# Performance work log

Measured on AMD Instinct MI355X. Metric: run time of the kernel, lower is better.

The kernel has to match this reference:

```python
import jax, jax.numpy as jnp
import numpy as np

BATCH, SEQ, DIM, HEADS, DSTATE, BLOCK = 2, 4096, 1024, 16, 64, 64
LN_EPS = 1e-6

def segsum(x):
    # x: (..., T) -> (..., T, T); segsum[i, j] = sum_{j < k <= i} x[k]; -inf above diagonal
    T = x.shape[-1]
    cs = jnp.cumsum(x, axis=-1)
    seg = cs[..., :, None] - cs[..., None, :]
    mask = jnp.tril(jnp.ones((T, T), dtype=bool))
    return jnp.where(mask, seg, -jnp.inf)

def ssd_minimal_discrete(X, A, C, B, block_len):
    # X: (b,s,h,p) already multiplied by dt; A: (b,s,h) = A*dt; C readout, B input: (b,s,h,n)
    b, s, h, p = X.shape
    n = B.shape[-1]
    c = s // block_len
    l = block_len
    Xc = X.reshape(b, c, l, h, p)
    Bc = B.reshape(b, c, l, h, n)
    Cc = C.reshape(b, c, l, h, n)
    Ac = A.reshape(b, c, l, h).transpose(0, 3, 1, 2)  # (b,h,c,l)
    A_cumsum = jnp.cumsum(Ac, axis=-1)
    # 1. intra-chunk (diagonal block) outputs
    L = jnp.exp(segsum(Ac))  # (b,h,c,l,l)
    Y_diag = jnp.einsum('bclhn,bcshn,bhcls,bcshp->bclhp', Cc, Bc, L, Xc)
    # 2. states at end of each chunk
    decay_states = jnp.exp(A_cumsum[..., -1:] - A_cumsum)
    states = jnp.einsum('bclhn,bhcl,bclhp->bchpn', Bc, decay_states, Xc)
    # 3. inter-chunk recurrence on chunk states
    init = jnp.zeros_like(states[:, :1])
    states = jnp.concatenate([init, states], axis=1)  # (b,c+1,h,p,n)
    decay_chunk = jnp.exp(segsum(jnp.pad(A_cumsum[..., -1], ((0, 0), (0, 0), (1, 0)))))
    new_states = jnp.einsum('bhzc,bchpn->bzhpn', decay_chunk, states)
    states, final_state = new_states[:, :-1], new_states[:, -1]
    # 4. state -> output contribution (off-diagonal blocks)
    state_decay_out = jnp.exp(A_cumsum)
    Y_off = jnp.einsum('bclhn,bchpn,bhcl->bclhp', Cc, states, state_decay_out)
    return (Y_diag + Y_off).reshape(b, s, h, p), final_state

def setup_inputs():
    key = jax.random.key(0)
    ks = jax.random.split(key, 8)
    X = jax.random.normal(ks[0], (BATCH, SEQ, DIM), jnp.float32)
    B = jax.random.normal(ks[1], (BATCH, SEQ, HEADS * DSTATE), jnp.float32)
    C = jax.random.normal(ks[2], (BATCH, SEQ, HEADS * DSTATE), jnp.float32)
    W_dt = jax.random.normal(ks[3], (DIM, HEADS), jnp.float32) * 0.02
    # dt_bias initializer: inverse-softplus of dt ~ LogUniform(1e-3, 1e-1)
    dt = jnp.exp(jax.random.uniform(ks[4], (1, SEQ, HEADS)) * (jnp.log(0.1) - jnp.log(0.001)) + jnp.log(0.001))
    dt = jnp.clip(dt, 1e-4)
    dt_bias = dt + jnp.log(-jnp.expm1(-dt))
    # a_log initializer: log of Uniform(1, 16)
    a_log = jnp.log(jax.random.uniform(ks[5], (HEADS,), minval=1.0, maxval=16.0))
    W_out = jax.random.normal(ks[6], (DIM, DIM), jnp.float32) * 0.02
    ln_scale = jnp.ones((DIM,), jnp.float32)
    ln_bias = jnp.zeros((DIM,), jnp.float32)
    return {"X": X, "B": B, "C": C, "W_dt": W_dt, "dt_bias": dt_bias, "a_log": a_log,
            "W_out": W_out, "ln_scale": ln_scale, "ln_bias": ln_bias, "block_len": BLOCK}

def reference(X, B, C, W_dt, dt_bias, a_log, W_out, ln_scale, ln_bias, block_len):
    b, s, dim = X.shape
    h = a_log.shape[0]
    Xh = X.reshape(b, s, h, -1)
    Bh = B.reshape(b, s, h, -1)
    Ch = C.reshape(b, s, h, -1)
    dt = jax.nn.softplus(jnp.einsum('bsd,dh->bsh', X, W_dt) + dt_bias)  # (b,s,h)
    A = -jnp.exp(a_log)  # (h,)
    y, final_state = ssd_minimal_discrete(Xh * dt[..., None], A * dt, Ch, Bh, block_len)
    y = y.reshape(b, s, dim)
    mu = jnp.mean(y, axis=-1, keepdims=True)
    var = jnp.mean(jnp.square(y - mu), axis=-1, keepdims=True)
    yn = (y - mu) / jnp.sqrt(var + LN_EPS) * ln_scale + ln_bias
    out = jnp.einsum('bsd,de->bse', yn, W_out)
    return out, final_state
```

## Files before the change

kernel.cpp:

```cpp
#include <hip/hip_runtime.h>
#include <hip/hip_bf16.h>
#include <hip/hip_fp16.h>
#include <math.h>

#define BATCH   2
#define SEQ     4096
#define DIM     1024
#define HEADS   16
#define DSTATE  64
#define HEADDIM 64
#define BLOCKL  64
#define NCHUNK  64
#define ROWS    (BATCH*SEQ)

typedef __attribute__((ext_vector_type(4))) float f32x4;
typedef __attribute__((ext_vector_type(8))) short bf16x8;
typedef __attribute__((ext_vector_type(8))) _Float16 f16x8;

static __device__ __forceinline__ float softplus_f(float x){
    return (x > 20.f) ? x : log1pf(__expf(x));
}
static __device__ __forceinline__ ushort f2b(float f){
    __hip_bfloat16 h = __float2bfloat16(f);
    return *reinterpret_cast<ushort*>(&h);
}
static __device__ __forceinline__ float b2f(ushort u){
    uint x = ((uint)u) << 16;
    return *reinterpret_cast<float*>(&x);
}
static __device__ __forceinline__ void gload16(const void* g, void* l){
    __builtin_amdgcn_global_load_lds((const __attribute__((address_space(1))) unsigned int*)g,
                                     (__attribute__((address_space(3))) unsigned int*)l, 16, 0, 0);
}

__global__ __launch_bounds__(256) void k_dtwt(const float* __restrict__ X,
        const float* __restrict__ Wdt, const float* __restrict__ dtb,
        const float* __restrict__ alog, const float* __restrict__ W,
        float* __restrict__ dt_g, float* __restrict__ dtA_g,
        ushort* __restrict__ Wt){
    __shared__ float xrow[DIM];
    __shared__ float red[16][17];
    __shared__ float t[64][65];
    int bidx = blockIdx.x;
    int tid = threadIdx.x;
    if (bidx < ROWS){
        int r = bidx;
        int s = r & (SEQ-1);
        *(f32x4*)(xrow + tid*4) = *(const f32x4*)(X + (size_t)r*DIM + tid*4);
        __syncthreads();
        int part = tid >> 4, h = tid & 15;
        int d0 = part * 64;
        float acc = 0.f;
        #pragma unroll 8
        for (int i = 0; i < 64; ++i)
            acc += xrow[d0 + i] * Wdt[(size_t)(d0 + i)*HEADS + h];
        red[part][h] = acc;
        __syncthreads();
        if (tid < 16){
            float sum = 0.f;
            #pragma unroll
            for (int p = 0; p < 16; ++p) sum += red[p][tid];
            sum += dtb[(size_t)s*HEADS + tid];
            float dtv = softplus_f(sum);
            dt_g[(size_t)r*HEADS + tid]  = dtv;
            dtA_g[(size_t)r*HEADS + tid] = -__expf(alog[tid]) * dtv;
        }
    } else {
        int bid = bidx - ROWS;
        int kt = bid >> 4, nt = bid & 15;
        int lr = tid >> 4, lc4 = (tid & 15) * 4;
        #pragma unroll
        for (int q = 0; q < 4; ++q){
            int k = lr + q*16;
            *(f32x4*)&t[k][lc4] = *(const f32x4*)(W + (size_t)(kt*64 + k)*DIM + nt*64 + lc4);
        }
        __syncthreads();
        #pragma unroll
        for (int q = 0; q < 4; ++q){
            int n = lr + q*16;
            ushort o[4];
            #pragma unroll
            for (int j = 0; j < 4; ++j) o[j] = f2b(t[lc4+j][n]);
            *(short4*)(Wt + (size_t)(nt*64 + n)*DIM + kt*64 + lc4) = *(short4*)&o[0];
        }
    }
}

__global__ __launch_bounds__(256) void k_chunk(const float* __restrict__ X,
        const float* __restrict__ Bin, const float* __restrict__ Cin,
        const float* __restrict__ dt_g, const float* __restrict__ dtA_g,
        ushort* __restrict__ ybf, ushort* __restrict__ cstate, float* __restrict__ css_g){
    int bid = blockIdx.x;
    int h = bid & 15, c = (bid >> 4) & 63, b = bid >> 10;
    int tid = threadIdx.x;
    int lane = tid & 63, wave = tid >> 6;
    int r0 = b*SEQ + c*BLOCKL;

    __shared__ __align__(16) char region0[18432];
    __shared__ __align__(16) ushort WBT[64*72];
    __shared__ float csh[64], dtsh[64], wsh[64];
    ushort* Cs  = (ushort*)region0;
    ushort* Bs  = (ushort*)(region0 + 9216);
    ushort* Mb  = (ushort*)region0;
    ushort* XdT = (ushort*)(region0 + 9216);

    int l  = tid >> 2;
    int c0 = (tid & 3) * 16;

    f32x4 xr[4], br[4], cr[4];
    {
        const float* xp = X   + (size_t)(r0 + l)*DIM + h*HEADDIM + c0;
        const float* bp = Bin + (size_t)(r0 + l)*DIM + h*DSTATE  + c0;
        const float* cp = Cin + (size_t)(r0 + l)*DIM + h*DSTATE  + c0;
        #pragma unroll
        for (int q = 0; q < 4; ++q){
            xr[q] = *(const f32x4*)(xp + q*4);
            br[q] = *(const f32x4*)(bp + q*4);
            cr[q] = *(const f32x4*)(cp + q*4);
        }
    }
    if (tid < 64){
        dtsh[tid] = dt_g[(size_t)(r0 + tid)*HEADS + h];
        float a = dtA_g[(size_t)(r0 + tid)*HEADS + h];
        #pragma unroll
        for (int off = 1; off < 64; off <<= 1){
            float v = __shfl_up(a, off, 64);
            if (tid >= off) a += v;
        }
        csh[tid] = a;
        css_g[(size_t)bid*64 + tid] = a;
        float cs63 = __shfl(a, 63, 64);
        wsh[tid] = __expf(cs63 - a);
    }
    {
        ushort tc[16], tb[16];
        #pragma unroll
        for (int q = 0; q < 4; ++q)
            #pragma unroll
            for (int j = 0; j < 4; ++j){
                tc[q*4+j] = f2b(cr[q][j]);
                tb[q*4+j] = f2b(br[q][j]);
            }
        *(uint4*)&Cs[l*72 + c0]     = *(uint4*)&tc[0];
        *(uint4*)&Cs[l*72 + c0 + 8] = *(uint4*)&tc[8];
        *(uint4*)&Bs[l*72 + c0]     = *(uint4*)&tb[0];
        *(uint4*)&Bs[l*72 + c0 + 8] = *(uint4*)&tb[8];
    }
    __syncthreads();

    int cl15  = lane & 15;
    int g     = lane >> 4;
    int arow  = wave*16 + cl15;
    int kof   = g * 8;
    int rbase = wave*16 + g*4;

    {
        float wl = wsh[l];
        #pragma unroll
        for (int q = 0; q < 4; ++q)
            #pragma unroll
            for (int j = 0; j < 4; ++j)
                WBT[(c0 + q*4 + j)*72 + l] = f2b(br[q][j] * wl);
    }
    f32x4 gacc[4];
    #pragma unroll
    for (int j = 0; j < 4; ++j) gacc[j] = (f32x4){0.f,0.f,0.f,0.f};
    #pragma unroll
    for (int k = 0; k < 2; ++k){
        bf16x8 a = *(const bf16x8*)&Cs[arow*72 + k*32 + kof];
        #pragma unroll
        for (int j = 0; j < 4; ++j){
            bf16x8 bb = *(const bf16x8*)&Bs[(16*j + cl15)*72 + k*32 + kof];
            gacc[j] = __builtin_amdgcn_mfma_f32_16x16x32_bf16(a, bb, gacc[j], 0, 0, 0);
        }
    }
    __syncthreads();

    #pragma unroll
    for (int j = 0; j < 4; ++j){
        #pragma unroll
        for (int r = 0; r < 4; ++r){
            int row = rbase + r, col = 16*j + cl15;
            float m = 0.f;
            if (col <= row) m = gacc[j][r] * __expf(csh[row] - csh[col]);
            Mb[row*72 + col] = f2b(m);
        }
    }
    {
        float dl = dtsh[l];
        #pragma unroll
        for (int q = 0; q < 4; ++q)
            #pragma unroll
            for (int j = 0; j < 4; ++j)
                XdT[(c0 + q*4 + j)*72 + l] = f2b(xr[q][j] * dl);
    }
    __syncthreads();

    f32x4 y[4];
    #pragma unroll
    for (int j = 0; j < 4; ++j) y[j] = (f32x4){0.f,0.f,0.f,0.f};
    #pragma unroll
    for (int k = 0; k < 2; ++k){
        bf16x8 am = *(const bf16x8*)&Mb[arow*72 + k*32 + kof];
        #pragma unroll
        for (int j = 0; j < 4; ++j){
            bf16x8 bx = *(const bf16x8*)&XdT[(16*j + cl15)*72 + k*32 + kof];
            y[j] = __builtin_amdgcn_mfma_f32_16x16x32_bf16(am, bx, y[j], 0, 0, 0);
        }
    }
    #pragma unroll
    for (int j = 0; j < 4; ++j)
        #pragma unroll
        for (int r = 0; r < 4; ++r)
            ybf[(size_t)(r0 + rbase + r)*DIM + h*HEADDIM + 16*j + cl15] = f2b(y[j][r]);

    f32x4 st[4];
    #pragma unroll
    for (int j = 0; j < 4; ++j) st[j] = (f32x4){0.f,0.f,0.f,0.f};
    #pragma unroll
    for (int k = 0; k < 2; ++k){
        bf16x8 aw = *(const bf16x8*)&XdT[arow*72 + k*32 + kof];
        #pragma unroll
        for (int j = 0; j < 4; ++j){
            bf16x8 bb = *(const bf16x8*)&WBT[(16*j + cl15)*72 + k*32 + kof];
            st[j] = __builtin_amdgcn_mfma_f32_16x16x32_bf16(aw, bb, st[j], 0, 0, 0);
        }
    }
    #pragma unroll
    for (int j = 0; j < 4; ++j)
        #pragma unroll
        for (int r = 0; r < 4; ++r){
            __half hv = __float2half(st[j][r]);
            cstate[(size_t)bid*4096 + (size_t)(rbase + r)*64 + 16*j + cl15] = *(ushort*)&hv;
        }
}

__global__ __launch_bounds__(256) void k_scan(ushort* __restrict__ cstate,
        const float* __restrict__ css_g, float* __restrict__ fs_out){
    int bid = blockIdx.x;
    int tile = bid & 7, hh = (bid >> 3) & 15, b = bid >> 7;
    int pn = tile*512 + threadIdx.x*2;
    size_t base0 = (size_t)(b*NCHUNK)*HEADS + hh;
    float P0 = 0.f, P1 = 0.f;
    __half2 cur = *(const __half2*)&cstate[base0*4096 + pn];
    for (int c = 0; c < NCHUNK; ++c){
        size_t base = base0 + (size_t)c*HEADS;
        __half2 nxt = cur;
        if (c < NCHUNK-1) nxt = *(const __half2*)&cstate[(base + HEADS)*4096 + pn];
        float e = __expf(css_g[base*64 + 63]);
        *( __half2*)&cstate[base*4096 + pn] = __floats2half2_rn(P0, P1);
        float2 cf = __half22float2(cur);
        P0 = e*P0 + cf.x;
        P1 = e*P1 + cf.y;
        cur = nxt;
    }
    *(float2*)&fs_out[(size_t)(b*HEADS + hh)*4096 + pn] = make_float2(P0, P1);
}

__global__ __launch_bounds__(256) void k_yoff(const float* __restrict__ Cin,
        const ushort* __restrict__ cstate, const float* __restrict__ css_g,
        ushort* __restrict__ ybf){
    int bid = blockIdx.x;
    int h = bid & 15, c = (bid >> 4) & 63, b = bid >> 10;
    int tid = threadIdx.x;
    int lane = tid & 63, wave = tid >> 6;
    int r0 = b*SEQ + c*BLOCKL;
    __shared__ __align__(16) ushort Cs[64*72];
    __shared__ __align__(16) ushort Ss[64*72];
    __shared__ float cse[64];
    {
        int l  = tid >> 2;
        int c0 = (tid & 3) * 16;
        const float* cp = Cin + (size_t)(r0 + l)*DIM + h*DSTATE + c0;
        ushort tc[16];
        #pragma unroll
        for (int q = 0; q < 4; ++q){
            f32x4 vc = *(const f32x4*)(cp + q*4);
            #pragma unroll
            for (int j = 0; j < 4; ++j){
                __half hv = __float2half(vc[j]);
                tc[q*4+j] = *(ushort*)&hv;
            }
        }
        *(uint4*)&Cs[l*72 + c0]     = *(uint4*)&tc[0];
        *(uint4*)&Cs[l*72 + c0 + 8] = *(uint4*)&tc[8];
        const ushort* sp = cstate + (size_t)bid*4096 + (size_t)l*64 + c0;
        *(uint4*)&Ss[l*72 + c0]     = *(const uint4*)sp;
        *(uint4*)&Ss[l*72 + c0 + 8] = *(const uint4*)(sp + 8);
    }
    if (tid < 64) cse[tid] = __expf(css_g[(size_t)bid*64 + tid]);
    __syncthreads();

    int cl15 = lane & 15;
    int g    = lane >> 4;
    int arow = wave*16 + cl15;
    int kof  = g * 8;
    f32x4 acc[4];
    #pragma unroll
    for (int j = 0; j < 4; ++j) acc[j] = (f32x4){0.f,0.f,0.f,0.f};
    #pragma unroll
    for (int k = 0; k < 2; ++k){
        f16x8 a = *(const f16x8*)&Cs[arow*72 + k*32 + kof];
        #pragma unroll
        for (int j = 0; j < 4; ++j){
            f16x8 bb = *(const f16x8*)&Ss[(16*j + cl15)*72 + k*32 + kof];
            acc[j] = __builtin_amdgcn_mfma_f32_16x16x32_f16(a, bb, acc[j], 0, 0, 0);
        }
    }
    int rbase = wave*16 + g*4;
    #pragma unroll
    for (int j = 0; j < 4; ++j)
        #pragma unroll
        for (int r = 0; r < 4; ++r){
            float e = cse[rbase + r];
            size_t idx = (size_t)(r0 + rbase + r)*DIM + h*HEADDIM + 16*j + cl15;
            ybf[idx] = f2b(b2f(ybf[idx]) + e * acc[j][r]);
        }
}

__global__ __launch_bounds__(256) void k_ln(ushort* __restrict__ ybf,
        const float* __restrict__ scale, const float* __restrict__ bias){
    int r = blockIdx.x, tid = threadIdx.x;
    ushort* yp = ybf + (size_t)r*DIM + tid*4;
    short4 raw = *(const short4*)yp;
    float v[4];
    v[0] = b2f((ushort)raw.x); v[1] = b2f((ushort)raw.y);
    v[2] = b2f((ushort)raw.z); v[3] = b2f((ushort)raw.w);
    float s1 = v[0]+v[1]+v[2]+v[3];
    float s2 = v[0]*v[0]+v[1]*v[1]+v[2]*v[2]+v[3]*v[3];
    #pragma unroll
    for (int m = 32; m > 0; m >>= 1){
        s1 += __shfl_xor(s1, m, 64);
        s2 += __shfl_xor(s2, m, 64);
    }
    __shared__ float w1[4], w2[4];
    int wv = tid >> 6;
    if ((tid & 63) == 0){ w1[wv] = s1; w2[wv] = s2; }
    __syncthreads();
    float S1 = w1[0]+w1[1]+w1[2]+w1[3];
    float S2 = w2[0]+w2[1]+w2[2]+w2[3];
    float mu  = S1 * (1.f/DIM);
    float var = S2 * (1.f/DIM) - mu*mu;
    float rstd = rsqrtf(var + 1e-6f);
    int d = tid*4;
    f32x4 sc = *(const f32x4*)(scale + d);
    f32x4 bi = *(const f32x4*)(bias + d);
    ushort o[4];
    #pragma unroll
    for (int j = 0; j < 4; ++j)
        o[j] = f2b((v[j] - mu)*rstd*sc[j] + bi[j]);
    *(short4*)yp = *(short4*)&o[0];
}

__global__ __launch_bounds__(256) void k_gemm(const ushort* __restrict__ A,
        const ushort* __restrict__ Bt, float* __restrict__ Out){
    __shared__ __align__(16) ushort As[128*32];
    __shared__ __align__(16) ushort Bsh[128*32];
    int bid = blockIdx.x;
    int wgid = (bid & 7)*64 + (bid >> 3);
    int bn = wgid & 7, bm = wgid >> 3;
    int tid = threadIdx.x;
    int lane = tid & 63, wave = tid >> 6;
    int wr = wave >> 1, wc = wave & 1;
    f32x4 acc[4][4];
    #pragma unroll
    for (int i = 0; i < 4; ++i)
        #pragma unroll
        for (int j = 0; j < 4; ++j)
            acc[i][j] = (f32x4){0.f, 0.f, 0.f, 0.f};
    const ushort* Ag = A  + (size_t)bm*128*1024;
    const ushort* Bg = Bt + (size_t)bn*128*1024;
    int row0 = tid >> 2;
    int col0 = (tid & 3) * 8;
    for (int k0 = 0; k0 < 1024; k0 += 32){
        const ushort* sA = Ag + (size_t)row0*1024 + k0 + col0;
        const ushort* sB = Bg + (size_t)row0*1024 + k0 + col0;
        gload16(sA,           &As[row0*32 + col0]);
        gload16(sA + 64*1024, &As[(row0+64)*32 + col0]);
        gload16(sB,           &Bsh[row0*32 + col0]);
        gload16(sB + 64*1024, &Bsh[(row0+64)*32 + col0]);
        __syncthreads();
        bf16x8 af[4], bfr[4];
        #pragma unroll
        for (int i = 0; i < 4; ++i){
            int arow = wr*64 + i*16 + (lane & 15);
            af[i] = *(const bf16x8*)&As[arow*32 + ((lane >> 4) << 3)];
        }
        #pragma unroll
        for (int j = 0; j < 4; ++j){
            int brow = wc*64 + j*16 + (lane & 15);
            bfr[j] = *(const bf16x8*)&Bsh[brow*32 + ((lane >> 4) << 3)];
        }
        #pragma unroll
        for (int i = 0; i < 4; ++i)
            #pragma unroll
            for (int j = 0; j < 4; ++j)
                acc[i][j] = __builtin_amdgcn_mfma_f32_16x16x32_bf16(af[i], bfr[j], acc[i][j], 0, 0, 0);
        __syncthreads();
    }
    #pragma unroll
    for (int i = 0; i < 4; ++i){
        int m0 = bm*128 + wr*64 + i*16 + ((lane >> 4) << 2);
        #pragma unroll
        for (int j = 0; j < 4; ++j){
            int n = bn*128 + wc*64 + j*16 + (lane & 15);
            #pragma unroll
            for (int reg = 0; reg < 4; ++reg)
                Out[(size_t)(m0 + reg)*1024 + n] = acc[i][j][reg];
        }
    }
}

extern "C" void kernel_launch(void* const* d_in, const int* in_sizes, int n_in,
                              void* d_out, int out_size, void* d_ws, size_t ws_size,
                              hipStream_t stream){
    const float* X    = (const float*)d_in[0];
    const float* Bin  = (const float*)d_in[1];
    const float* Cin  = (const float*)d_in[2];
    const float* Wdt  = (const float*)d_in[3];
    const float* dtb  = (const float*)d_in[4];
    const float* alog = (const float*)d_in[5];
    const float* Wout = (const float*)d_in[6];
    const float* lns  = (const float*)d_in[7];
    const float* lnb  = (const float*)d_in[8];

    float* out = (float*)d_out;
    float* fs_out = out + (size_t)ROWS*DIM;

    char* ws = (char*)d_ws;
    float*  dt_g   = (float*)(ws);
    float*  dtA_g  = (float*)(ws + 524288);
    float*  css_g  = (float*)(ws + 1048576);
    ushort* cstate = (ushort*)(ws + 1572864);
    ushort* ybf    = (ushort*)(ws + 18350080);
    ushort* Wt     = (ushort*)(ws + 35127296);

    k_dtwt <<<ROWS + 256,         256, 0, stream>>>(X, Wdt, dtb, alog, Wout, dt_g, dtA_g, Wt);
    k_chunk<<<BATCH*NCHUNK*HEADS, 256, 0, stream>>>(X, Bin, Cin, dt_g, dtA_g, ybf, cstate, css_g);
    k_scan <<<BATCH*HEADS*8,      256, 0, stream>>>(cstate, css_g, fs_out);
    k_yoff <<<BATCH*NCHUNK*HEADS, 256, 0, stream>>>(Cin, cstate, css_g, ybf);
    k_ln   <<<ROWS,               256, 0, stream>>>(ybf, lns, lnb);
    k_gemm <<<512,                256, 0, stream>>>(ybf, Wt, out);
}
```

Measured before the change: 123.0 us.

## Shrink k_chunk LDS via shuffles and region reuse; prefetch scan two ahead

In k_chunk, per-row dt and cumsum values now stay in registers of every wave and are read with shuffles instead of shared arrays. WBT and Mb now alias the freed B-tile region, which cuts LDS use to raise occupancy, and the state and intra-chunk matmuls are reordered to fit that aliasing, at the cost of an extra barrier. In k_scan, the per-chunk decay exponentials are computed once into shared memory, and state loads are prefetched two chunks ahead to hide load latency in the serial recurrence.

New measurement: 122.7 us. No clear change (-0.3%).

```diff
diff --git a/kernel.cpp b/kernel.cpp
--- a/kernel.cpp
+++ b/kernel.cpp
@@ -97,12 +97,11 @@
     int r0 = b*SEQ + c*BLOCKL;
 
     __shared__ __align__(16) char region0[18432];
-    __shared__ __align__(16) ushort WBT[64*72];
-    __shared__ float csh[64], dtsh[64], wsh[64];
     ushort* Cs  = (ushort*)region0;
     ushort* Bs  = (ushort*)(region0 + 9216);
-    ushort* Mb  = (ushort*)region0;
-    ushort* XdT = (ushort*)(region0 + 9216);
+    ushort* XdT = (ushort*)region0;
+    ushort* WBT = (ushort*)(region0 + 9216);
+    ushort* Mb  = (ushort*)(region0 + 9216);
 
     int l  = tid >> 2;
     int c0 = (tid & 3) * 16;
@@ -119,19 +118,17 @@
             cr[q] = *(const f32x4*)(cp + q*4);
         }
     }
-    if (tid < 64){
-        dtsh[tid] = dt_g[(size_t)(r0 + tid)*HEADS + h];
-        float a = dtA_g[(size_t)(r0 + tid)*HEADS + h];
-        #pragma unroll
-        for (int off = 1; off < 64; off <<= 1){
-            float v = __shfl_up(a, off, 64);
-            if (tid >= off) a += v;
-        }
-        csh[tid] = a;
-        css_g[(size_t)bid*64 + tid] = a;
-        float cs63 = __shfl(a, 63, 64);
-        wsh[tid] = __expf(cs63 - a);
-    }
+    float dt_l = dt_g[(size_t)(r0 + lane)*HEADS + h];
+    float a    = dtA_g[(size_t)(r0 + lane)*HEADS + h];
+    #pragma unroll
+    for (int off = 1; off < 64; off <<= 1){
+        float v = __shfl_up(a, off, 64);
+        if (lane >= off) a += v;
+    }
+    float cs63 = __shfl(a, 63, 64);
+    float w_l  = __expf(cs63 - a);
+    if (tid < 64) css_g[(size_t)bid*64 + tid] = a;
+
     {
         ushort tc[16], tb[16];
         #pragma unroll
@@ -154,65 +151,33 @@
     int kof   = g * 8;
     int rbase = wave*16 + g*4;
 
+    f32x4 gacc[4];
+    #pragma unroll
+    for (int j = 0; j < 4; ++j) gacc[j] = (f32x4){0.f,0.f,0.f,0.f};
+    #pragma unroll
+    for (int k = 0; k < 2; ++k){
+        bf16x8 aa = *(const bf16x8*)&Cs[arow*72 + k*32 + kof];
+        #pragma unroll
+        for (int j = 0; j < 4; ++j){
+            bf16x8 bb = *(const bf16x8*)&Bs[(16*j + cl15)*72 + k*32 + kof];
+            gacc[j] = __builtin_amdgcn_mfma_f32_16x16x32_bf16(aa, bb, gacc[j], 0, 0, 0);
+        }
+    }
+    __syncthreads();
+
     {
-        float wl = wsh[l];
+        float dl = __shfl(dt_l, l, 64);
+        float wl = __shfl(w_l,  l, 64);
         #pragma unroll
         for (int q = 0; q < 4; ++q)
             #pragma unroll
-            for (int j = 0; j < 4; ++j)
-                WBT[(c0 + q*4 + j)*72 + l] = f2b(br[q][j] * wl);
-    }
-    f32x4 gacc[4];
-    #pragma unroll
-    for (int j = 0; j < 4; ++j) gacc[j] = (f32x4){0.f,0.f,0.f,0.f};
-    #pragma unroll
-    for (int k = 0; k < 2; ++k){
-        bf16x8 a = *(const bf16x8*)&Cs[arow*72 + k*32 + kof];
-        #pragma unroll
-        for (int j = 0; j < 4; ++j){
-            bf16x8 bb = *(const bf16x8*)&Bs[(16*j + cl15)*72 + k*32 + kof];
-            gacc[j] = __builtin_amdgcn_mfma_f32_16x16x32_bf16(a, bb, gacc[j], 0, 0, 0);
-        }
-    }
-    __syncthreads();
-
-    #pragma unroll
-    for (int j = 0; j < 4; ++j){
-        #pragma unroll
-        for (int r = 0; r < 4; ++r){
-            int row = rbase + r, col = 16*j + cl15;
-            float m = 0.f;
-            if (col <= row) m = gacc[j][r] * __expf(csh[row] - csh[col]);
-            Mb[row*72 + col] = f2b(m);
-        }
-    }
-    {
-        float dl = dtsh[l];
-        #pragma unroll
-        for (int q = 0; q < 4; ++q)
-            #pragma unroll
-            for (int j = 0; j < 4; ++j)
-                XdT[(c0 + q*4 + j)*72 + l] = f2b(xr[q][j] * dl);
-    }
-    __syncthreads();
-
-    f32x4 y[4];
-    #pragma unroll
-    for (int j = 0; j < 4; ++j) y[j] = (f32x4){0.f,0.f,0.f,0.f};
-    #pragma unroll
-    for (int k = 0; k < 2; ++k){
-        bf16x8 am = *(const bf16x8*)&Mb[arow*72 + k*32 + kof];
-        #pragma unroll
-        for (int j = 0; j < 4; ++j){
-            bf16x8 bx = *(const bf16x8*)&XdT[(16*j + cl15)*72 + k*32 + kof];
-            y[j] = __builtin_amdgcn_mfma_f32_16x16x32_bf16(am, bx, y[j], 0, 0, 0);
-        }
-    }
-    #pragma unroll
-    for (int j = 0; j < 4; ++j)
-        #pragma unroll
-        for (int r = 0; r < 4; ++r)
-            ybf[(size_t)(r0 + rbase + r)*DIM + h*HEADDIM + 16*j + cl15] = f2b(y[j][r]);
+            for (int j = 0; j < 4; ++j){
+                int p = c0 + q*4 + j;
+                XdT[p*72 + l] = f2b(xr[q][j] * dl);
+                WBT[p*72 + l] = f2b(br[q][j] * wl);
+            }
+    }
+    __syncthreads();
 
     f32x4 st[4];
     #pragma unroll
@@ -233,26 +198,76 @@
             __half hv = __float2half(st[j][r]);
             cstate[(size_t)bid*4096 + (size_t)(rbase + r)*64 + 16*j + cl15] = *(ushort*)&hv;
         }
+
+    float mreg[4][4];
+    {
+        float csr[4], csc[4];
+        #pragma unroll
+        for (int r = 0; r < 4; ++r) csr[r] = __shfl(a, rbase + r, 64);
+        #pragma unroll
+        for (int j = 0; j < 4; ++j) csc[j] = __shfl(a, 16*j + cl15, 64);
+        #pragma unroll
+        for (int j = 0; j < 4; ++j)
+            #pragma unroll
+            for (int r = 0; r < 4; ++r){
+                int row = rbase + r, col = 16*j + cl15;
+                mreg[j][r] = (col <= row) ? gacc[j][r]*__expf(csr[r] - csc[j]) : 0.f;
+            }
+    }
+    __syncthreads();
+
+    #pragma unroll
+    for (int j = 0; j < 4; ++j)
+        #pragma unroll
+        for (int r = 0; r < 4; ++r)
+            Mb[(rbase + r)*72 + 16*j + cl15] = f2b(mreg[j][r]);
+    __syncthreads();
+
+    f32x4 y[4];
+    #pragma unroll
+    for (int j = 0; j < 4; ++j) y[j] = (f32x4){0.f,0.f,0.f,0.f};
+    #pragma unroll
+    for (int k = 0; k < 2; ++k){
+        bf16x8 am = *(const bf16x8*)&Mb[arow*72 + k*32 + kof];
+        #pragma unroll
+        for (int j = 0; j < 4; ++j){
+            bf16x8 bx = *(const bf16x8*)&XdT[(16*j + cl15)*72 + k*32 + kof];
+            y[j] = __builtin_amdgcn_mfma_f32_16x16x32_bf16(am, bx, y[j], 0, 0, 0);
+        }
+    }
+    #pragma unroll
+    for (int j = 0; j < 4; ++j)
+        #pragma unroll
+        for (int r = 0; r < 4; ++r)
+            ybf[(size_t)(r0 + rbase + r)*DIM + h*HEADDIM + 16*j + cl15] = f2b(y[j][r]);
 }
 
 __global__ __launch_bounds__(256) void k_scan(ushort* __restrict__ cstate,
         const float* __restrict__ css_g, float* __restrict__ fs_out){
     int bid = blockIdx.x;
     int tile = bid & 7, hh = (bid >> 3) & 15, b = bid >> 7;
-    int pn = tile*512 + threadIdx.x*2;
+    int tid = threadIdx.x;
+    int pn = tile*512 + tid*2;
     size_t base0 = (size_t)(b*NCHUNK)*HEADS + hh;
+    __shared__ float esh[64];
+    if (tid < 64)
+        esh[tid] = __expf(css_g[(base0 + (size_t)tid*HEADS)*64 + 63]);
+    __syncthreads();
+    ushort* p0 = cstate + base0*4096 + pn;
+    const size_t cstep = (size_t)HEADS*4096;
     float P0 = 0.f, P1 = 0.f;
-    __half2 cur = *(const __half2*)&cstate[base0*4096 + pn];
+    __half2 cur = *(const __half2*)p0;
+    __half2 nxt = *(const __half2*)(p0 + cstep);
     for (int c = 0; c < NCHUNK; ++c){
-        size_t base = base0 + (size_t)c*HEADS;
-        __half2 nxt = cur;
-        if (c < NCHUNK-1) nxt = *(const __half2*)&cstate[(base + HEADS)*4096 + pn];
-        float e = __expf(css_g[base*64 + 63]);
-        *( __half2*)&cstate[base*4096 + pn] = __floats2half2_rn(P0, P1);
+        __half2 fut = nxt;
+        if (c + 2 < NCHUNK) fut = *(const __half2*)(p0 + (size_t)(c+2)*cstep);
+        *( __half2*)(p0 + (size_t)c*cstep) = __floats2half2_rn(P0, P1);
         float2 cf = __half22float2(cur);
+        float e = esh[c];
         P0 = e*P0 + cf.x;
         P1 = e*P1 + cf.y;
         cur = nxt;
+        nxt = fut;
     }
     *(float2*)&fs_out[(size_t)(b*HEADS + hh)*4096 + pn] = make_float2(P0, P1);
 }
```
